# Kernel tuning notes

Measured on AMD Instinct MI355X. Metric: run time of the kernel, lower is better.

## Reference

```python
import jax, jax.numpy as jnp
import numpy as np

B = 128
NHEAD = 16
D_MODEL = 512
D_IN = 256  # each of f_* and f_*_out; concat -> 512
N_ATOM = 128


def _scopes():
    lens = np.array([96 + (i % 33) for i in range(B)], dtype=np.int64)  # max == 128 == N_ATOM
    starts_a = np.concatenate([[1], 1 + np.cumsum(lens)[:-1]]).astype(np.int64)
    nb = 2 * lens
    starts_b = np.concatenate([[1], 1 + np.cumsum(nb)[:-1]]).astype(np.int64)
    return lens, starts_a, nb, starts_b


def setup_inputs() -> dict:
    key = jax.random.key(0)
    ks = jax.random.split(key, 10)
    lens, starts_a, nb, starts_b = _scopes()
    Na = int(1 + lens.sum())   # 14279 (row 0 is padding)
    Nb = int(1 + nb.sum())     # 28557 (bond 0 is padding)
    f_atoms = jax.random.normal(ks[0], (Na, D_IN), jnp.float32)
    f_bonds = jax.random.normal(ks[1], (Nb, D_IN), jnp.float32)
    f_atoms_out = jax.random.normal(ks[2], (Na, D_IN), jnp.float32)
    f_bonds_out = jax.random.normal(ks[3], (Nb, D_IN), jnp.float32)
    b2a = jax.random.randint(ks[4], (Nb,), 0, 96, jnp.int64 if jax.config.jax_enable_x64 else jnp.int32)
    b2revb = jax.random.randint(ks[5], (Nb,), 0, Nb, b2a.dtype)
    a_scope = jnp.stack([jnp.asarray(starts_a), jnp.asarray(lens)], axis=1)
    b_scope = jnp.stack([jnp.asarray(starts_b), jnp.asarray(nb)], axis=1)
    W_atom = jax.random.normal(ks[6], (2 * D_IN, D_MODEL), jnp.float32) * 0.02
    b_atom = jnp.zeros((D_MODEL,), jnp.float32)
    W_bond = jax.random.normal(ks[7], (2 * D_IN, NHEAD), jnp.float32) * 0.02
    b_bond = jnp.zeros((NHEAD,), jnp.float32)
    return {"f_atoms": f_atoms, "f_bonds": f_bonds, "f_atoms_out": f_atoms_out,
            "f_bonds_out": f_bonds_out, "b2a": b2a, "b2revb": b2revb,
            "a_scope": a_scope, "b_scope": b_scope, "n_atom": N_ATOM,
            "W_atom": W_atom, "b_atom": b_atom, "W_bond": W_bond, "b_bond": b_bond}


def reference(f_atoms, f_bonds, f_atoms_out, f_bonds_out, b2a, b2revb,
              a_scope, b_scope, n_atom, W_atom, b_atom, W_bond, b_bond):
    Bsz = a_scope.shape[0]
    # atom embedding: concat + linear, drop padding row 0, pad per-molecule -> [n_atom, B, d]
    atoms = jnp.concatenate([f_atoms, f_atoms_out], axis=1) @ W_atom + b_atom  # [Na, d]
    starts_a, lens_a = a_scope[:, 0], a_scope[:, 1]
    pos = jnp.arange(n_atom)
    valid = pos[None, :] < lens_a[:, None]                       # [B, n_atom]
    gidx = jnp.where(valid, starts_a[:, None] + pos[None, :], 0)  # safe gather idx
    atoms_pad = jnp.where(valid[..., None], atoms[gidx], 0.0)     # [B, n_atom, d]
    atoms_emb = atoms_pad.transpose(1, 0, 2)                      # [n_atom, B, d] (batch_first=False)
    # bond embedding -> scatter into dense pairwise matrix
    bonds = jnp.concatenate([f_bonds, f_bonds_out], axis=1) @ W_bond + b_bond  # [Nb, nhead]
    Nb = bonds.shape[0]
    starts_b = b_scope[:, 0]
    mol = jnp.searchsorted(starts_b, jnp.arange(Nb), side='right') - 1  # molecule id per bond (-1 for pad bond 0)
    offset = jnp.maximum(mol, 0) * (n_atom * n_atom)
    idx = b2a + b2a[b2revb] * n_atom + offset                     # flat index into [B*n_atom*n_atom]
    flat = jnp.zeros((Bsz * n_atom * n_atom, bonds.shape[1]), bonds.dtype).at[idx].set(bonds)
    apairs = flat.reshape(Bsz, n_atom, n_atom, -1)                # [B, n_atom, n_atom, nhead]
    padding_mask = ~valid                                         # [B, n_atom], True = pad
    apairs = jnp.where(padding_mask[:, None, :, None], -jnp.inf, apairs)
    apairs = apairs.transpose(0, 3, 1, 2)                         # [B, nhead, n_atom, n_atom]
    return atoms_emb, apairs, padding_mask
```

## Files before the change

kernel.cpp:

```cpp
#include <hip/hip_runtime.h>
#include <math.h>

#define NEG_BIG (-1e30f)

typedef __attribute__((ext_vector_type(8))) short short8;
typedef __attribute__((ext_vector_type(8))) _Float16 half8;
typedef __attribute__((ext_vector_type(4))) float floatx4;

__device__ __forceinline__ unsigned short f2bf(float x) {
    unsigned u = __float_as_uint(x);
    unsigned r = (u + 0x7fffu + ((u >> 16) & 1u)) >> 16;
    return (unsigned short)r;
}
__device__ __forceinline__ short f2h(float x) {
    _Float16 h = (_Float16)x;
    return __builtin_bit_cast(short, h);
}
__device__ __forceinline__ float h2f(short s) {
    return (float)__builtin_bit_cast(_Float16, s);
}


__device__ __forceinline__ void bonds_body(
    int bbid, char* smem,
    const float* __restrict__ fB, const float* __restrict__ fBo,
    const float* __restrict__ Wb_raw, const float* __restrict__ bb_,
    float* __restrict__ bonds, int Nb)
{
    short* feat = (short*)smem;
    short* wb   = (short*)(smem + 17408);

    const int tid = threadIdx.x;
    const int j0 = bbid * 64;

    for (int c = tid; c < 8192; c += 256) {
        int k = c >> 4, h = c & 15;
        wb[h * 512 + ((((k >> 3) + h) & 63) << 3) + (k & 7)] = (short)f2bf(Wb_raw[c]);
    }

    const int wid = tid >> 6, lane = tid & 63;
    const int quad = lane >> 4, l16 = lane & 15;
    floatx4 acc = (floatx4){0.f, 0.f, 0.f, 0.f};

    const int fr = tid >> 2;
    const int fs = (tid & 3) * 32;
    const int j = j0 + fr;

    for (int k0 = 0; k0 < 512; k0 += 128) {
        float x[32];
        if (j < Nb) {
            const float* p = (k0 < 256) ? (fB + (size_t)j * 256 + k0 + fs)
                                        : (fBo + (size_t)j * 256 + (k0 - 256) + fs);
#pragma unroll
            for (int i = 0; i < 8; i++) {
                float4 v = ((const float4*)p)[i];
                x[i * 4 + 0] = v.x; x[i * 4 + 1] = v.y;
                x[i * 4 + 2] = v.z; x[i * 4 + 3] = v.w;
            }
        } else {
#pragma unroll
            for (int i = 0; i < 32; i++) x[i] = 0.f;
        }
        __syncthreads();
#pragma unroll
        for (int c = 0; c < 4; c++) {
            short8 s;
#pragma unroll
            for (int i = 0; i < 8; i++) s[i] = (short)f2bf(x[c * 8 + i]);
            *(short8*)&feat[fr * 136 + fs + c * 8] = s;
        }
        __syncthreads();
#pragma unroll
        for (int kk = 0; kk < 4; kk++) {
            short8 a = *(const short8*)&feat[(wid * 16 + l16) * 136 + kk * 32 + quad * 8];
            int kchunk = (k0 + kk * 32 + quad * 8) >> 3;
            short8 b = *(const short8*)&wb[l16 * 512 + (((kchunk + l16) & 63) * 8)];
            acc = __builtin_amdgcn_mfma_f32_16x16x32_bf16(a, b, acc, 0, 0, 0);
        }
    }
    float bv = bb_[l16];
#pragma unroll
    for (int r = 0; r < 4; r++) {
        int jj = j0 + wid * 16 + quad * 4 + r;
        if (jj < Nb) bonds[(size_t)jj * 16 + l16] = acc[r] + bv;
    }
}

__device__ __forceinline__ void scatter_body(
    int sbid, char* smem,
    const int* __restrict__ b2a, const int* __restrict__ b2revb,
    const int* __restrict__ b_scope, int* __restrict__ winner,
    int Nb, int Bmol)
{
    int* sb = (int*)smem;
    int tid = threadIdx.x;
    if (tid < Bmol) sb[tid] = b_scope[2 * tid];
    __syncthreads();
    int j = sbid * 256 + tid;
    if (j >= Nb) return;
    int lo = 0, hi = Bmol;
    while (lo < hi) { int mid = (lo + hi) >> 1; if (sb[mid] <= j) lo = mid + 1; else hi = mid; }
    int mol = lo - 1; if (mol < 0) mol = 0;
    int p2 = b2a[j];
    int p1 = b2a[b2revb[j]];
    atomicMax(&winner[mol * 16384 + p1 * 128 + p2], j);
}

__device__ __forceinline__ void atoms_body(
    int abid, char* smem,
    const float* __restrict__ fA, const float* __restrict__ fAo,
    const int* __restrict__ a_scope,
    const short* __restrict__ WH, const short* __restrict__ WL,
    const float* __restrict__ bias, float* __restrict__ out, int Bmol)
{
    short* A_s = (short*)smem;
    short* B_s = (short*)(smem + 20480);
    int*   rs  = (int*)(smem + 40960);

    const int tid = threadIdx.x;
    const int n0 = (abid & 3) * 128;
    const int mol = abid >> 2;

    if (tid < 128) {
        int len = a_scope[2 * mol + 1];
        rs[tid] = (tid < len) ? (a_scope[2 * mol] + tid) : -1;
    }
    const int wid = tid >> 6, lane = tid & 63;
    const int wm = (wid >> 1) * 64, wn = (wid & 1) * 64;
    const int quad = lane >> 4, l16 = lane & 15;

    floatx4 acc1[4][4], acc2[4][4];
#pragma unroll
    for (int i = 0; i < 4; i++)
#pragma unroll
        for (int j = 0; j < 4; j++) {
            acc1[i][j] = (floatx4){0.f, 0.f, 0.f, 0.f};
            acc2[i][j] = (floatx4){0.f, 0.f, 0.f, 0.f};
        }

    const int ar = tid >> 1;
    const int ak = (tid & 1) * 16;
    __syncthreads();
    const int asrc = rs[ar];

    for (int k0 = 0; k0 < 512; k0 += 32) {
        float x[16];
        if (asrc >= 0) {
            int kg = k0 + ak;
            const float* p = (kg < 256) ? (fA + (size_t)asrc * 256 + kg)
                                        : (fAo + (size_t)asrc * 256 + (kg - 256));
#pragma unroll
            for (int i = 0; i < 4; i++) {
                float4 v = ((const float4*)p)[i];
                x[i * 4 + 0] = v.x; x[i * 4 + 1] = v.y;
                x[i * 4 + 2] = v.z; x[i * 4 + 3] = v.w;
            }
        } else {
#pragma unroll
            for (int i = 0; i < 16; i++) x[i] = 0.f;
        }
        size_t goff = (size_t)(n0 + ar) * 512 + k0 + ak;
        short8 bh0 = *(const short8*)(WH + goff);
        short8 bh1 = *(const short8*)(WH + goff + 8);
        short8 bl0 = *(const short8*)(WL + goff);
        short8 bl1 = *(const short8*)(WL + goff + 8);

        short8 ah0, ah1, al0, al1;
#pragma unroll
        for (int i = 0; i < 8; i++) {
            short h = f2h(x[i]);
            float r = (x[i] - h2f(h)) * 2048.0f;
            ah0[i] = h; al0[i] = f2h(r);
        }
#pragma unroll
        for (int i = 0; i < 8; i++) {
            float xx = x[8 + i];
            short h = f2h(xx);
            float r = (xx - h2f(h)) * 2048.0f;
            ah1[i] = h; al1[i] = f2h(r);
        }

        __syncthreads();
        const int abase = ar * 40 + ak;
        *(short8*)&A_s[abase] = ah0;          *(short8*)&A_s[abase + 8] = ah1;
        *(short8*)&A_s[5120 + abase] = al0;   *(short8*)&A_s[5120 + abase + 8] = al1;
        *(short8*)&B_s[abase] = bh0;          *(short8*)&B_s[abase + 8] = bh1;
        *(short8*)&B_s[5120 + abase] = bl0;   *(short8*)&B_s[5120 + abase + 8] = bl1;
        __syncthreads();

        half8 afh[4], afl[4];
#pragma unroll
        for (int ti = 0; ti < 4; ti++) {
            int off = (wm + ti * 16 + l16) * 40 + quad * 8;
            afh[ti] = *(const half8*)&A_s[off];
            afl[ti] = *(const half8*)&A_s[5120 + off];
        }
#pragma unroll
        for (int tj = 0; tj < 4; tj++) {
            int off = (wn + tj * 16 + l16) * 40 + quad * 8;
            half8 bh = *(const half8*)&B_s[off];
            half8 bl = *(const half8*)&B_s[5120 + off];
#pragma unroll
            for (int ti = 0; ti < 4; ti++) {
                acc1[ti][tj] = __builtin_amdgcn_mfma_f32_16x16x32_f16(afh[ti], bh, acc1[ti][tj], 0, 0, 0);
                acc2[ti][tj] = __builtin_amdgcn_mfma_f32_16x16x32_f16(afh[ti], bl, acc2[ti][tj], 0, 0, 0);
                acc2[ti][tj] = __builtin_amdgcn_mfma_f32_16x16x32_f16(afl[ti], bh, acc2[ti][tj], 0, 0, 0);
            }
        }
    }

#pragma unroll
    for (int tj = 0; tj < 4; tj++) {
        int n = n0 + wn + tj * 16 + l16;
        float bv = bias[n];
#pragma unroll
        for (int ti = 0; ti < 4; ti++) {
#pragma unroll
            for (int r = 0; r < 4; r++) {
                int pos = wm + ti * 16 + quad * 4 + r;
                bool valid = rs[pos] >= 0;
                float v = valid ? (acc1[ti][tj][r] + 4.8828125e-4f * acc2[ti][tj][r] + bv) : 0.f;
                out[((size_t)pos * Bmol + mol) * 512 + n] = v;
            }
        }
    }
}

__device__ __forceinline__ void fill_body(
    int fbid, const int* __restrict__ a_scope, float* __restrict__ out_ap)
{
    int f = fbid * 256 + threadIdx.x;
    int r = f >> 3;
    int b = r >> 11;
    int p2b = (f & 7) * 16;
    int len = a_scope[2 * b + 1];
    float4* dst = (float4*)(out_ap + (size_t)f * 16);
#pragma unroll
    for (int c = 0; c < 4; c++) {
        float4 v;
        v.x = (p2b + c * 4 + 0 >= len) ? NEG_BIG : 0.f;
        v.y = (p2b + c * 4 + 1 >= len) ? NEG_BIG : 0.f;
        v.z = (p2b + c * 4 + 2 >= len) ? NEG_BIG : 0.f;
        v.w = (p2b + c * 4 + 3 >= len) ? NEG_BIG : 0.f;
        dst[c] = v;
    }
}

__global__ __launch_bounds__(256) void k_phase1(
    const float* __restrict__ fB, const float* __restrict__ fBo,
    const float* __restrict__ Wb_raw, const float* __restrict__ b_bond,
    float* __restrict__ bonds_ws, int Nb,
    const float* __restrict__ W, short* __restrict__ WH, short* __restrict__ WL,
    const int* __restrict__ b2a, const int* __restrict__ b2revb,
    const int* __restrict__ b_scope, int* __restrict__ winner,
    const int* __restrict__ a_scope, float* __restrict__ mask_out,
    int Bmol, int nBondsB, int nScatB)
{
    __shared__ char smem[33792];
    int bid = blockIdx.x;
    int tid = threadIdx.x;
    if (bid < nBondsB) {
        bonds_body(bid, smem, fB, fBo, Wb_raw, b_bond, bonds_ws, Nb);
        return;
    }
    bid -= nBondsB;
    if (bid < 1024) {
        int t = bid * 256 + tid;
        int n = t >> 9, k = t & 511;
        float x = W[(size_t)k * 512 + n];
        short h = f2h(x);
        float r = (x - h2f(h)) * 2048.0f;
        WH[t] = h;
        WL[t] = f2h(r);
        return;
    }
    bid -= 1024;
    if (bid < nScatB) {
        scatter_body(bid, smem, b2a, b2revb, b_scope, winner, Nb, Bmol);
        return;
    }
    bid -= nScatB;
    {
        int t = bid * 256 + tid;
        if (t < Bmol * 128) {
            int b = t >> 7, p = t & 127;
            mask_out[t] = (p >= a_scope[2 * b + 1]) ? 1.0f : 0.0f;
        }
    }
}

__global__ __launch_bounds__(256, 2) void k_phase2(
    const float* __restrict__ fA, const float* __restrict__ fAo,
    const int* __restrict__ a_scope,
    const short* __restrict__ WH, const short* __restrict__ WL,
    const float* __restrict__ b_atom,
    float* __restrict__ out_emb, float* __restrict__ out_ap,
    int Bmol, int nAtomsB)
{
    __shared__ char smem[41472];
    int bid = blockIdx.x;
    if (bid < nAtomsB) {
        atoms_body(bid, smem, fA, fAo, a_scope, WH, WL, b_atom, out_emb, Bmol);
        return;
    }
    fill_body(bid - nAtomsB, a_scope, out_ap);
}

__global__ __launch_bounds__(256) void k_commit(
    const int* __restrict__ b2a, const int* __restrict__ b2revb,
    const int* __restrict__ b_scope, const int* __restrict__ a_scope,
    const int* __restrict__ winner, const float* __restrict__ bonds,
    float* __restrict__ out_ap, int Nb, int Bmol)
{
    __shared__ int sb[128];
    int tid = threadIdx.x;
    if (tid < Bmol) sb[tid] = b_scope[2 * tid];
    __syncthreads();
    int t = blockIdx.x * 256 + tid;
    int j = t >> 4, h = t & 15;
    if (j >= Nb) return;
    int lo = 0, hi = Bmol;
    while (lo < hi) { int mid = (lo + hi) >> 1; if (sb[mid] <= j) lo = mid + 1; else hi = mid; }
    int mol = lo - 1; if (mol < 0) mol = 0;
    int p2 = b2a[j];
    int p1 = b2a[b2revb[j]];
    int cell = mol * 16384 + p1 * 128 + p2;
    if (winner[cell] != j) return;
    if (p2 >= a_scope[2 * mol + 1]) return;
    out_ap[(((size_t)mol * 16 + h) * 128 + p1) * 128 + p2] = bonds[(size_t)j * 16 + h];
}

extern "C" void kernel_launch(void* const* d_in, const int* in_sizes, int n_in,
                              void* d_out, int out_size, void* d_ws, size_t ws_size,
                              hipStream_t stream)
{
    const float* f_atoms     = (const float*)d_in[0];
    const float* f_bonds     = (const float*)d_in[1];
    const float* f_atoms_out = (const float*)d_in[2];
    const float* f_bonds_out = (const float*)d_in[3];
    const int*   b2a         = (const int*)d_in[4];
    const int*   b2revb      = (const int*)d_in[5];
    const int*   a_scope     = (const int*)d_in[6];
    const int*   b_scope     = (const int*)d_in[7];
    const float* W_atom      = (const float*)d_in[9];
    const float* b_atom      = (const float*)d_in[10];
    const float* W_bond      = (const float*)d_in[11];
    const float* b_bond      = (const float*)d_in[12];

    const int Bmol = in_sizes[6] / 2;
    const int Nb   = in_sizes[4];

    char* ws = (char*)d_ws;
    size_t off = 0;
    float* bonds_ws = (float*)(ws + off); off += ((size_t)Nb * 16 * 4 + 255) & ~(size_t)255;
    int*   winner   = (int*)(ws + off);   off += (size_t)Bmol * 16384 * 4;
    short* WH       = (short*)(ws + off); off += 512 * 512 * 2;
    short* WL       = (short*)(ws + off); off += 512 * 512 * 2;

    float* out_emb  = (float*)d_out;
    float* out_ap   = out_emb + (size_t)128 * Bmol * 512;
    float* out_mask = out_ap + (size_t)Bmol * 16 * 128 * 128;

    hipMemsetAsync(winner, 0xFF, (size_t)Bmol * 16384 * 4, stream);

    const int nBondsB = (Nb + 63) / 64;
    const int nScatB  = (Nb + 255) / 256;
    const int nMaskB  = (Bmol * 128 + 255) / 256;
    hipLaunchKernelGGL(k_phase1, dim3(nBondsB + 1024 + nScatB + nMaskB), dim3(256), 0, stream,
                       f_bonds, f_bonds_out, W_bond, b_bond, bonds_ws, Nb,
                       W_atom, WH, WL,
                       b2a, b2revb, b_scope, winner,
                       a_scope, out_mask, Bmol, nBondsB, nScatB);

    const int nAtomsB = 4 * Bmol;
    const int nFillB  = Bmol * 64;
    hipLaunchKernelGGL(k_phase2, dim3(nAtomsB + nFillB), dim3(256), 0, stream,
                       f_atoms, f_atoms_out, a_scope, WH, WL, b_atom,
                       out_emb, out_ap, Bmol, nAtomsB);

    hipLaunchKernelGGL(k_commit, dim3((Nb * 16 + 255) / 256), dim3(256), 0, stream,
                       b2a, b2revb, b_scope, a_scope, winner, bonds_ws, out_ap, Nb, Bmol);
}
```

Measured before the change: 334.0 us.

## Build dense apairs by per-cell winner gather fused into atoms kernel

```diff
diff --git a/kernel.cpp b/kernel.cpp
--- a/kernel.cpp
+++ b/kernel.cpp
@@ -226,23 +226,69 @@
     }
 }
 
-__device__ __forceinline__ void fill_body(
-    int fbid, const int* __restrict__ a_scope, float* __restrict__ out_ap)
-{
-    int f = fbid * 256 + threadIdx.x;
-    int r = f >> 3;
-    int b = r >> 11;
-    int p2b = (f & 7) * 16;
+__device__ __forceinline__ void apairs_body(
+    int chunk, const int* __restrict__ winner, const float* __restrict__ bonds,
+    const int* __restrict__ a_scope, float* __restrict__ out_ap)
+{
+    int t = chunk * 256 + threadIdx.x;
+    int b = t >> 12;
+    int p1 = (t >> 5) & 127;
+    int p2q = t & 31;
     int len = a_scope[2 * b + 1];
-    float4* dst = (float4*)(out_ap + (size_t)f * 16);
-#pragma unroll
-    for (int c = 0; c < 4; c++) {
+    const int4 w = ((const int4*)winner)[t];
+
+    int wi0 = w.x, wi1 = w.y, wi2 = w.z, wi3 = w.w;
+    float rows[4][16];
+#pragma unroll
+    for (int c = 0; c < 16; c++) {
+        rows[0][c] = 0.f; rows[1][c] = 0.f; rows[2][c] = 0.f; rows[3][c] = 0.f;
+    }
+    if (wi0 >= 0) {
+        const float4* p = (const float4*)(bonds + (size_t)wi0 * 16);
+#pragma unroll
+        for (int c = 0; c < 4; c++) {
+            float4 v = p[c];
+            rows[0][4*c+0] = v.x; rows[0][4*c+1] = v.y; rows[0][4*c+2] = v.z; rows[0][4*c+3] = v.w;
+        }
+    }
+    if (wi1 >= 0) {
+        const float4* p = (const float4*)(bonds + (size_t)wi1 * 16);
+#pragma unroll
+        for (int c = 0; c < 4; c++) {
+            float4 v = p[c];
+            rows[1][4*c+0] = v.x; rows[1][4*c+1] = v.y; rows[1][4*c+2] = v.z; rows[1][4*c+3] = v.w;
+        }
+    }
+    if (wi2 >= 0) {
+        const float4* p = (const float4*)(bonds + (size_t)wi2 * 16);
+#pragma unroll
+        for (int c = 0; c < 4; c++) {
+            float4 v = p[c];
+            rows[2][4*c+0] = v.x; rows[2][4*c+1] = v.y; rows[2][4*c+2] = v.z; rows[2][4*c+3] = v.w;
+        }
+    }
+    if (wi3 >= 0) {
+        const float4* p = (const float4*)(bonds + (size_t)wi3 * 16);
+#pragma unroll
+        for (int c = 0; c < 4; c++) {
+            float4 v = p[c];
+            rows[3][4*c+0] = v.x; rows[3][4*c+1] = v.y; rows[3][4*c+2] = v.z; rows[3][4*c+3] = v.w;
+        }
+    }
+
+    bool iv0 = (p2q * 4 + 0 >= len);
+    bool iv1 = (p2q * 4 + 1 >= len);
+    bool iv2 = (p2q * 4 + 2 >= len);
+    bool iv3 = (p2q * 4 + 3 >= len);
+    float* ob = out_ap + ((size_t)b * 16 * 128 + p1) * 128 + p2q * 4;
+#pragma unroll
+    for (int h = 0; h < 16; h++) {
         float4 v;
-        v.x = (p2b + c * 4 + 0 >= len) ? NEG_BIG : 0.f;
-        v.y = (p2b + c * 4 + 1 >= len) ? NEG_BIG : 0.f;
-        v.z = (p2b + c * 4 + 2 >= len) ? NEG_BIG : 0.f;
-        v.w = (p2b + c * 4 + 3 >= len) ? NEG_BIG : 0.f;
-        dst[c] = v;
+        v.x = iv0 ? NEG_BIG : rows[0][h];
+        v.y = iv1 ? NEG_BIG : rows[1][h];
+        v.z = iv2 ? NEG_BIG : rows[2][h];
+        v.w = iv3 ? NEG_BIG : rows[3][h];
+        *(float4*)(ob + (size_t)h * 16384) = v;
     }
 }
 
@@ -294,40 +340,23 @@
     const int* __restrict__ a_scope,
     const short* __restrict__ WH, const short* __restrict__ WL,
     const float* __restrict__ b_atom,
+    const int* __restrict__ winner, const float* __restrict__ bonds_ws,
     float* __restrict__ out_emb, float* __restrict__ out_ap,
-    int Bmol, int nAtomsB)
+    int Bmol)
 {
     __shared__ char smem[41472];
-    int bid = blockIdx.x;
-    if (bid < nAtomsB) {
-        atoms_body(bid, smem, fA, fAo, a_scope, WH, WL, b_atom, out_emb, Bmol);
-        return;
-    }
-    fill_body(bid - nAtomsB, a_scope, out_ap);
-}
-
-__global__ __launch_bounds__(256) void k_commit(
-    const int* __restrict__ b2a, const int* __restrict__ b2revb,
-    const int* __restrict__ b_scope, const int* __restrict__ a_scope,
-    const int* __restrict__ winner, const float* __restrict__ bonds,
-    float* __restrict__ out_ap, int Nb, int Bmol)
-{
-    __shared__ int sb[128];
-    int tid = threadIdx.x;
-    if (tid < Bmol) sb[tid] = b_scope[2 * tid];
-    __syncthreads();
-    int t = blockIdx.x * 256 + tid;
-    int j = t >> 4, h = t & 15;
-    if (j >= Nb) return;
-    int lo = 0, hi = Bmol;
-    while (lo < hi) { int mid = (lo + hi) >> 1; if (sb[mid] <= j) lo = mid + 1; else hi = mid; }
-    int mol = lo - 1; if (mol < 0) mol = 0;
-    int p2 = b2a[j];
-    int p1 = b2a[b2revb[j]];
-    int cell = mol * 16384 + p1 * 128 + p2;
-    if (winner[cell] != j) return;
-    if (p2 >= a_scope[2 * mol + 1]) return;
-    out_ap[(((size_t)mol * 16 + h) * 128 + p1) * 128 + p2] = bonds[(size_t)j * 16 + h];
+    const int bid = blockIdx.x;
+    const int s = bid & 3;
+    int ai = 0;
+#pragma unroll
+    for (int r = 0; r < 5; r++) {
+        if (r == s) {
+            atoms_body(bid, smem, fA, fAo, a_scope, WH, WL, b_atom, out_emb, Bmol);
+        } else {
+            apairs_body(bid * 4 + ai, winner, bonds_ws, a_scope, out_ap);
+            ai++;
+        }
+    }
 }
 
 extern "C" void kernel_launch(void* const* d_in, const int* in_sizes, int n_in,
@@ -372,12 +401,7 @@
                        b2a, b2revb, b_scope, winner,
                        a_scope, out_mask, Bmol, nBondsB, nScatB);
 
-    const int nAtomsB = 4 * Bmol;
-    const int nFillB  = Bmol * 64;
-    hipLaunchKernelGGL(k_phase2, dim3(nAtomsB + nFillB), dim3(256), 0, stream,
+    hipLaunchKernelGGL(k_phase2, dim3(4 * Bmol), dim3(256), 0, stream,
                        f_atoms, f_atoms_out, a_scope, WH, WL, b_atom,
-                       out_emb, out_ap, Bmol, nAtomsB);
-
-    hipLaunchKernelGGL(k_commit, dim3((Nb * 16 + 255) / 256), dim3(256), 0, stream,
-                       b2a, b2revb, b_scope, a_scope, winner, bonds_ws, out_ap, Nb, Bmol);
-}
+                       winner, bonds_ws, out_emb, out_ap, Bmol);
+}
```

New measurement: 299.4 us. 1.12x faster.
